# Performance work log

Hardware: AMD Instinct MI355X
Metric: run time of the kernel (lower is better)

The kernel has to match this reference:

```python
import jax, jax.numpy as jnp
import numpy as np
from jax import lax

B, S, T = 64, 64, 32
VE = VD = 32000
E = H = 256
L = 2


def _cell(x, h, c, Wih, Whh, b):
    # PyTorch LSTM gate order: i, f, g, o
    g = x @ Wih.T + h @ Whh.T + b  # [B, 4H]
    i, f, gg, o = jnp.split(g, 4, axis=-1)
    c2 = jax.nn.sigmoid(f) * c + jax.nn.sigmoid(i) * jnp.tanh(gg)
    h2 = jax.nn.sigmoid(o) * jnp.tanh(c2)
    return h2, c2


def _stack_step(x, h, c, Wih, Whh, b):
    # x: [B, E]; h, c: [L, B, H]. Stacked LSTM, dropout is identity at inference.
    hs, cs = [], []
    inp = x
    for l in range(h.shape[0]):
        h2, c2 = _cell(inp, h[l], c[l], Wih[l], Whh[l], b[l])
        hs.append(h2); cs.append(c2)
        inp = h2
    return jnp.stack(hs), jnp.stack(cs), inp


def _encode(tokens, emb, Wih, Whh, b):
    x = emb[tokens]  # [B, S, E]
    bsz = tokens.shape[0]
    h0 = jnp.zeros((L, bsz, H), x.dtype)
    c0 = jnp.zeros((L, bsz, H), x.dtype)

    def step(carry, xt):
        h, c = carry
        h, c, _ = _stack_step(xt, h, c, Wih, Whh, b)
        return (h, c), None

    (h, c), _ = lax.scan(step, (h0, c0), x.transpose(1, 0, 2))
    return h, c


def setup_inputs():
    key = jax.random.key(0)
    ks = jax.random.split(key, 12)
    sd = lambda k, shape: (jax.random.normal(k, shape, dtype=jnp.float32) * 0.05)
    return {
        "input_seq": jax.random.randint(ks[0], (B, S), 0, VE),
        "target_seq": jax.random.randint(ks[1], (B, T), 0, VD),
        "enc_emb": sd(ks[2], (VE, E)),
        "dec_emb": sd(ks[3], (VD, E)),
        "enc_Wih": sd(ks[4], (L, 4 * H, E)),
        "enc_Whh": sd(ks[5], (L, 4 * H, H)),
        "enc_b": sd(ks[6], (L, 4 * H)),
        "dec_Wih": sd(ks[7], (L, 4 * H, E)),
        "dec_Whh": sd(ks[8], (L, 4 * H, H)),
        "dec_b": sd(ks[9], (L, 4 * H)),
        "W_out": sd(ks[10], (VD, H)),
        "b_out": sd(ks[11], (VD,)),
    }


def reference(input_seq, target_seq, enc_emb, dec_emb, enc_Wih, enc_Whh, enc_b,
              dec_Wih, dec_Whh, dec_b, W_out, b_out):
    h, c = _encode(input_seq, enc_emb, enc_Wih, enc_Whh, enc_b)
    bsz, tlen = target_seq.shape
    # dec_in buffer; position 0 is BOS token target_seq[:, 0]; rest filled greedily
    buf0 = jnp.zeros((bsz, tlen), dtype=target_seq.dtype).at[:, 0].set(target_seq[:, 0])
    pos = jnp.arange(tlen)

    def outer(carry, t):
        h, c, buf = carry
        x = dec_emb[buf]  # [B, T, E] -- whole growing prefix re-fed, as in source

        def inner(carry, inp):
            hh, cc = carry
            xt, p = inp
            h2, c2, _ = _stack_step(xt, hh, cc, dec_Wih, dec_Whh, dec_b)
            m = p <= t  # only positions up to current prefix length update state
            hh = jnp.where(m, h2, hh)
            cc = jnp.where(m, c2, cc)
            return (hh, cc), None

        (h, c), _ = lax.scan(inner, (h, c), (x.transpose(1, 0, 2), pos))
        out_top = h[-1]  # LSTM output at last real position t
        pred = out_top @ W_out.T + b_out  # [B, V]
        nxt = jnp.argmax(pred, axis=-1).astype(buf.dtype)
        buf = buf.at[:, t + 1].set(nxt)
        return (h, c, buf), pred

    (_, _, _), preds = lax.scan(outer, (h, c, buf0), jnp.arange(tlen - 1))
    return preds.transpose(1, 0, 2)  # [B, T-1, V]
```

## Files before the change

kernel.cpp:

```cpp
#include <hip/hip_runtime.h>
#include <math.h>


#define B     64
#define SLEN  64
#define TLEN  32
#define HID   256
#define EMBD  256
#define G4    1024
#define VOC   32000
#define NPRED 31

typedef unsigned long long u64;

__device__ __forceinline__ float sigf(float x){ return 1.0f/(1.0f+__expf(-x)); }

__device__ __forceinline__ void gstoref(float* p, float v){
  __hip_atomic_store(p, v, __ATOMIC_RELAXED, __HIP_MEMORY_SCOPE_AGENT);
}
__device__ __forceinline__ void gstorei(int* p, int v){
  __hip_atomic_store(p, v, __ATOMIC_RELAXED, __HIP_MEMORY_SCOPE_AGENT);
}
__device__ __forceinline__ float gloadf(const float* p){
  return __hip_atomic_load(p, __ATOMIC_RELAXED, __HIP_MEMORY_SCOPE_AGENT);
}
__device__ __forceinline__ int gload32(const int* p){
  return __hip_atomic_load(p, __ATOMIC_RELAXED, __HIP_MEMORY_SCOPE_AGENT);
}

__global__ void k_init(const int* __restrict__ tgt, int* __restrict__ buf){
  int r = threadIdx.x;
  if (r < B) buf[r*TLEN] = tgt[r*TLEN];
}

__global__ void k_zero(int* __restrict__ p){
  if (threadIdx.x < 192) p[threadIdx.x] = 0;
}

__global__ __launch_bounds__(256) void k_tr(const float* __restrict__ src,
                                            float* __restrict__ dst){
  __shared__ float t[64][65];
  const int r0 = blockIdx.x*64, c0 = blockIdx.y*64;
  const int lr = threadIdx.x>>6, lc = threadIdx.x&63;
  #pragma unroll
  for (int i=0;i<16;i++){
    int r = lr + i*4;
    t[r][lc] = src[(size_t)(r0+r)*256 + c0+lc];
  }
  __syncthreads();
  #pragma unroll
  for (int i=0;i<16;i++){
    int c = lr + i*4;
    dst[(size_t)(c0+c)*1024 + r0+lc] = t[lc][c];
  }
}

__global__ __launch_bounds__(256) void k_xproj(
    const int* __restrict__ tok, int tok_stride, int pos0,
    const float* __restrict__ emb, const float* __restrict__ W,
    const float* __restrict__ b0, float* __restrict__ out)
{
  __shared__ float xT[128][64];
  const int tid  = threadIdx.x;
  const int lane = tid & 63;
  const int wv   = __builtin_amdgcn_readfirstlane(tid >> 6);
  const int pos  = pos0 + blockIdx.y;
  const int jbase= blockIdx.x*32 + wv*8;

  const int rS = tid >> 2, klane = tid & 3;
  const int tokrow = tok[rS*tok_stride + pos];
  const float* xsrc = emb + (size_t)tokrow*EMBD;

  float acc[8];
  #pragma unroll
  for (int jj=0;jj<8;jj++) acc[jj]=0.f;

  for (int c=0;c<2;c++){
    __syncthreads();
    #pragma unroll
    for (int i=0;i<32;i++){
      int k = klane + 4*i;
      xT[k][rS] = xsrc[c*128 + k];
    }
    __syncthreads();
    for (int kc=0;kc<8;kc++){
      float x[16];
      #pragma unroll
      for (int i=0;i<16;i++) x[i] = xT[kc*16+i][lane];
      #pragma unroll
      for (int jj=0;jj<8;jj++){
        const float* Wp = W + (size_t)(jbase+jj)*EMBD + c*128 + kc*16;
        float s = 0.f;
        #pragma unroll
        for (int i=0;i<16;i++) s += Wp[i]*x[i];
        acc[jj] += s;
      }
    }
  }
  #pragma unroll
  for (int jj=0;jj<8;jj++){
    int j = jbase+jj;
    out[((size_t)pos*G4 + j)*64 + lane] = acc[jj] + b0[j];
  }
}

__device__ __forceinline__ float4 dotpart(const float4* __restrict__ Wq,
                                          const float* __restrict__ hs,
                                          int kq, int jg){
  float ax=0.f, ay=0.f, az=0.f, aw=0.f;
  const float4* __restrict__ hq = (const float4*)(hs + (kq<<6));
  const float4* __restrict__ w  = Wq + (size_t)(kq<<6)*256 + jg;
  #pragma unroll 4
  for (int kk=0; kk<16; ++kk){
    float4 h4 = hq[kk];
    float4 w0 = w[0];
    float4 w1 = w[256];
    float4 w2 = w[512];
    float4 w3 = w[768];
    ax += w0.x*h4.x; ay += w0.y*h4.x; az += w0.z*h4.x; aw += w0.w*h4.x;
    ax += w1.x*h4.y; ay += w1.y*h4.y; az += w1.z*h4.y; aw += w1.w*h4.y;
    ax += w2.x*h4.z; ay += w2.y*h4.z; az += w2.z*h4.z; aw += w2.w*h4.z;
    ax += w3.x*h4.w; ay += w3.y*h4.w; az += w3.z*h4.w; aw += w3.w*h4.w;
    w += 1024;
  }
  return make_float4(ax,ay,az,aw);
}

__global__ __launch_bounds__(1024) void k_pipe(
    const float* __restrict__ xp, int nsteps,
    const float* __restrict__ WT0, const float* __restrict__ WT1i,
    const float* __restrict__ WT1h, const float* __restrict__ b1,
    float* __restrict__ h0P, float* __restrict__ h1P,
    float* __restrict__ c0P, float* __restrict__ c1P,
    float* __restrict__ h0R, float* __restrict__ p1R,
    int* __restrict__ fA, int* __restrict__ fB1, int* __restrict__ fB2,
    int fbase, int initzero)
{
  __shared__ __align__(16) float part[4][4096];
  __shared__ float xps[1024];
  __shared__ __align__(16) float hloc[256];
  __shared__ float padL[4096];
  const int tid  = threadIdx.x;
  const int kq   = tid >> 8, jg = tid & 255;
  const int role = blockIdx.x >> 6;
  const int r    = blockIdx.x & 63;
  if (nsteps < 0){ padL[tid] = xp[tid]; h0R[tid] = padL[tid ^ 1]; }

  if (role == 0){
    float c0 = 0.f;
    if (tid < HID){
      if (initzero){ c0 = 0.f; hloc[tid] = 0.f; }
      else { c0 = c0P[tid*64 + r]; hloc[tid] = h0P[tid*64 + r]; }
    }
    __syncthreads();
    const float4* W4 = (const float4*)WT0;
    for (int q = 0; q < nsteps; ++q){
      float xv = xp[((size_t)q*G4 + tid)*64 + r];
      if (tid == 0 && q >= 4){
        int tgt = fbase + q - 3, g = 0;
        while (gload32(fB1 + r) < tgt && ++g < (1<<24)) {}
      }
      xps[tid] = xv;
      float4 a = dotpart(W4, hloc, kq, jg);
      *(float4*)&part[kq][jg<<2] = a;
      __syncthreads();
      if (tid < HID){
        float g0 = part[0][tid]+part[1][tid]+part[2][tid]+part[3][tid] + xps[tid];
        float g1 = part[0][HID+tid]+part[1][HID+tid]+part[2][HID+tid]+part[3][HID+tid] + xps[HID+tid];
        float g2 = part[0][2*HID+tid]+part[1][2*HID+tid]+part[2][2*HID+tid]+part[3][2*HID+tid] + xps[2*HID+tid];
        float g3 = part[0][3*HID+tid]+part[1][3*HID+tid]+part[2][3*HID+tid]+part[3][3*HID+tid] + xps[3*HID+tid];
        c0 = sigf(g1)*c0 + sigf(g0)*tanhf(g2);
        float h = sigf(g3)*tanhf(c0);
        hloc[tid] = h;
        gstoref(h0R + (q&3)*16384 + r*256 + tid, h);
        asm volatile("s_waitcnt vmcnt(0)" ::: "memory");
      }
      __syncthreads();
      if (tid == 0) gstorei(fA + r, fbase + q + 1);
    }
    if (tid < HID){ c0P[tid*64 + r] = c0; h0P[tid*64 + r] = hloc[tid]; }
  }
  else if (role == 1){
    const float4* W4 = (const float4*)WT1i;
    for (int q = 0; q < nsteps; ++q){
      if (tid == 0){
        int tgt = fbase + q + 1, g = 0;
        while (gload32(fA + r) < tgt && ++g < (1<<24)) {}
        if (q >= 4){
          int t2 = fbase + q - 3; g = 0;
          while (gload32(fB2 + r) < t2 && ++g < (1<<24)) {}
        }
      }
      __syncthreads();
      if (tid < HID) hloc[tid] = gloadf(h0R + (q&3)*16384 + r*256 + tid);
      __syncthreads();
      float4 a = dotpart(W4, hloc, kq, jg);
      *(float4*)&part[kq][jg<<2] = a;
      __syncthreads();
      float p = part[0][tid]+part[1][tid]+part[2][tid]+part[3][tid];
      gstoref(p1R + (q&3)*65536 + r*1024 + tid, p);
      asm volatile("s_waitcnt vmcnt(0)" ::: "memory");
      __syncthreads();
      if (tid == 0) gstorei(fB1 + r, fbase + q + 1);
    }
  }
  else {
    float c1 = 0.f, bb0=0.f, bb1=0.f, bb2=0.f, bb3=0.f;
    if (tid < HID){
      bb0 = b1[tid]; bb1 = b1[HID+tid]; bb2 = b1[2*HID+tid]; bb3 = b1[3*HID+tid];
      if (initzero){ c1 = 0.f; hloc[tid] = 0.f; }
      else { c1 = c1P[tid*64 + r]; hloc[tid] = h1P[tid*64 + r]; }
    }
    __syncthreads();
    const float4* W4 = (const float4*)WT1h;
    for (int q = 0; q < nsteps; ++q){
      if (tid == 0){
        int tgt = fbase + q + 1, g = 0;
        while (gload32(fB1 + r) < tgt && ++g < (1<<24)) {}
      }
      __syncthreads();
      xps[tid] = gloadf(p1R + (q&3)*65536 + r*1024 + tid);
      asm volatile("s_waitcnt vmcnt(0)" ::: "memory");
      __syncthreads();
      if (tid == 0) gstorei(fB2 + r, fbase + q + 1);
      float4 a = dotpart(W4, hloc, kq, jg);
      *(float4*)&part[kq][jg<<2] = a;
      __syncthreads();
      if (tid < HID){
        float g0 = part[0][tid]+part[1][tid]+part[2][tid]+part[3][tid] + xps[tid] + bb0;
        float g1 = part[0][HID+tid]+part[1][HID+tid]+part[2][HID+tid]+part[3][HID+tid] + xps[HID+tid] + bb1;
        float g2 = part[0][2*HID+tid]+part[1][2*HID+tid]+part[2][2*HID+tid]+part[3][2*HID+tid] + xps[2*HID+tid] + bb2;
        float g3 = part[0][3*HID+tid]+part[1][3*HID+tid]+part[2][3*HID+tid]+part[3][3*HID+tid] + xps[3*HID+tid] + bb3;
        c1 = sigf(g1)*c1 + sigf(g0)*tanhf(g2);
        float h = sigf(g3)*tanhf(c1);
        hloc[tid] = h;
        if (q == nsteps-1) h1P[tid*64 + r] = h;
      }
      __syncthreads();
    }
    if (tid < HID) c1P[tid*64 + r] = c1;
  }
}

__global__ __launch_bounds__(256) void k_pred(
    const float* __restrict__ h1, const float* __restrict__ Wout,
    const float* __restrict__ bout, float* __restrict__ dout, int t,
    float* __restrict__ pval, int* __restrict__ pidx)
{
  __shared__ float xT[128][64];
  __shared__ float cval[4][64];
  __shared__ int   cidx[4][64];
  const int tid  = threadIdx.x;
  const int lane = tid & 63;
  const int wv   = __builtin_amdgcn_readfirstlane(tid >> 6);
  const int vbase= blockIdx.x*32 + wv*8;

  float acc[8];
  #pragma unroll
  for (int vv=0;vv<8;vv++) acc[vv]=0.f;

  for (int c=0;c<2;c++){
    __syncthreads();
    {
      const float4* s4 = (const float4*)(h1 + c*8192);
      float4* d4 = (float4*)&xT[0][0];
      #pragma unroll
      for (int i=0;i<8;i++) d4[tid + i*256] = s4[tid + i*256];
    }
    __syncthreads();
    for (int kc=0;kc<8;kc++){
      float x[16];
      #pragma unroll
      for (int i=0;i<16;i++) x[i] = xT[kc*16+i][lane];
      #pragma unroll
      for (int vv=0;vv<8;vv++){
        const float* Wp = Wout + (size_t)(vbase+vv)*HID + c*128 + kc*16;
        float s = 0.f;
        #pragma unroll
        for (int i=0;i<16;i++) s += Wp[i]*x[i];
        acc[vv] += s;
      }
    }
  }

  const int r = lane;
  float best = -INFINITY; int bi = 0;
  #pragma unroll
  for (int vv=0; vv<8; vv++){
    int v = vbase + vv;
    float val = acc[vv] + bout[v];
    dout[((size_t)r*NPRED + t)*VOC + v] = val;
    if (val > best){ best = val; bi = v; }
  }
  cval[wv][lane] = best; cidx[wv][lane] = bi;
  __syncthreads();
  if (tid < 64){
    float bb = cval[0][tid]; int bbi = cidx[0][tid];
    #pragma unroll
    for (int w=1; w<4; w++){
      float v = cval[w][tid];
      if (v > bb){ bb = v; bbi = cidx[w][tid]; }
    }
    pval[(size_t)tid*1024 + blockIdx.x] = bb;
    pidx[(size_t)tid*1024 + blockIdx.x] = bbi;
  }
}

__global__ __launch_bounds__(256) void k_amax(
    const float* __restrict__ pval, const int* __restrict__ pidx,
    int* __restrict__ buf, int t)
{
  __shared__ float sv[256]; __shared__ int si[256];
  const int r = blockIdx.x, tid = threadIdx.x;
  float best = -INFINITY; int bi = 0x7fffffff;
  for (int w = tid; w < 1000; w += 256){
    float v = pval[(size_t)r*1024 + w]; int ii = pidx[(size_t)r*1024 + w];
    if (v > best || (v == best && ii < bi)){ best = v; bi = ii; }
  }
  sv[tid] = best; si[tid] = bi;
  __syncthreads();
  for (int s2 = 128; s2 > 0; s2 >>= 1){
    if (tid < s2){
      float v = sv[tid+s2]; int ii = si[tid+s2];
      if (v > sv[tid] || (v == sv[tid] && ii < si[tid])){ sv[tid]=v; si[tid]=ii; }
    }
    __syncthreads();
  }
  if (tid == 0) buf[r*TLEN + t + 1] = si[0];
}

extern "C" void kernel_launch(void* const* d_in, const int* in_sizes, int n_in,
                              void* d_out, int out_size, void* d_ws, size_t ws_size,
                              hipStream_t stream)
{
  const int*   input_seq  = (const int*)d_in[0];
  const int*   target_seq = (const int*)d_in[1];
  const float* enc_emb = (const float*)d_in[2];
  const float* dec_emb = (const float*)d_in[3];
  const float* enc_Wih = (const float*)d_in[4];
  const float* enc_Whh = (const float*)d_in[5];
  const float* enc_b   = (const float*)d_in[6];
  const float* dec_Wih = (const float*)d_in[7];
  const float* dec_Whh = (const float*)d_in[8];
  const float* dec_b   = (const float*)d_in[9];
  const float* W_out   = (const float*)d_in[10];
  const float* b_out   = (const float*)d_in[11];
  float* out = (float*)d_out;

  float* ws   = (float*)d_ws;
  float* xp_e = ws;
  float* xp_d = xp_e + (size_t)SLEN*G4*64;
  float* h0P  = xp_d + (size_t)TLEN*G4*64;
  float* h1P  = h0P + HID*64;
  float* c0P  = h1P + HID*64;
  float* c1P  = c0P + HID*64;
  float* h0R  = c1P + HID*64;
  float* p1R  = h0R + 4*64*HID;
  float* pval = p1R + 4*64*G4;
  int*   pidx = (int*)(pval + (size_t)B*1024);
  int*   buf  = pidx + (size_t)B*1024;
  int*   fA   = buf + B*TLEN;
  int*   fB1  = fA + 64;
  int*   fB2  = fB1 + 64;
  float* WT0  = (float*)(fB2 + 64);
  float* WT1i = WT0  + HID*G4;
  float* WT1h = WT1i + HID*G4;

  k_init<<<1, 64, 0, stream>>>(target_seq, buf);
  k_zero<<<1, 256, 0, stream>>>(fA);

  dim3 trg(16, 4);
  k_tr<<<trg, 256, 0, stream>>>(enc_Whh,                   WT0);
  k_tr<<<trg, 256, 0, stream>>>(enc_Wih + (size_t)G4*EMBD, WT1i);
  k_tr<<<trg, 256, 0, stream>>>(enc_Whh + (size_t)G4*HID,  WT1h);
  k_xproj<<<dim3(32, SLEN), 256, 0, stream>>>(input_seq, SLEN, 0, enc_emb,
        enc_Wih, enc_b, xp_e);
  k_pipe<<<192, 1024, 0, stream>>>(xp_e, SLEN,
        WT0, WT1i, WT1h, enc_b + G4,
        h0P, h1P, c0P, c1P, h0R, p1R, fA, fB1, fB2, 0, 1);

  k_tr<<<trg, 256, 0, stream>>>(dec_Whh,                   WT0);
  k_tr<<<trg, 256, 0, stream>>>(dec_Wih + (size_t)G4*EMBD, WT1i);
  k_tr<<<trg, 256, 0, stream>>>(dec_Whh + (size_t)G4*HID,  WT1h);

  int fb = SLEN;
  for (int t = 0; t < NPRED; t++){
    k_xproj<<<dim3(32, 1), 256, 0, stream>>>(buf, TLEN, t, dec_emb,
        dec_Wih, dec_b, xp_d);
    k_pipe<<<192, 1024, 0, stream>>>(xp_d, t+1,
        WT0, WT1i, WT1h, dec_b + G4,
        h0P, h1P, c0P, c1P, h0R, p1R, fA, fB1, fB2, fb, 0);
    fb += t + 1;
    k_pred<<<1000, 256, 0, stream>>>(h1P, W_out, b_out, out, t, pval, pidx);
    k_amax<<<B, 256, 0, stream>>>(pval, pidx, buf, t);
  }
}
```

Baseline: 8.604 ms.

## Fuse entire greedy decode loop into one persistent multi-role kernel

Replaces the per-step host loop of xproj, pipe, pred and argmax launches with a single persistent kernel of 256 blocks split into four roles (layer-0 cell, layer-1 input projection, layer-1 cell, vocab projection with argmax and next-token embedding projection). The roles synchronise through global flag counters and ring buffers. This removes about 124 kernel launches and their serialisation, and lets the vocab projection for step t overlap with the recurrent work of step t+1. The cost is that vocab work now runs on 64 blocks instead of 1000, spin-wait synchronisation adds latency and deadlock risk, and all 256 large blocks must be co-resident.

```diff
diff --git a/kernel.cpp b/kernel.cpp
--- a/kernel.cpp
+++ b/kernel.cpp
@@ -10,6 +10,7 @@
 #define G4    1024
 #define VOC   32000
 #define NPRED 31
+#define FBASE 64
 
 typedef unsigned long long u64;
 
@@ -28,13 +29,8 @@
   return __hip_atomic_load(p, __ATOMIC_RELAXED, __HIP_MEMORY_SCOPE_AGENT);
 }
 
-__global__ void k_init(const int* __restrict__ tgt, int* __restrict__ buf){
-  int r = threadIdx.x;
-  if (r < B) buf[r*TLEN] = tgt[r*TLEN];
-}
-
 __global__ void k_zero(int* __restrict__ p){
-  if (threadIdx.x < 192) p[threadIdx.x] = 0;
+  p[threadIdx.x] = 0;
 }
 
 __global__ __launch_bounds__(256) void k_tr(const float* __restrict__ src,
@@ -242,91 +238,294 @@
   }
 }
 
-__global__ __launch_bounds__(256) void k_pred(
-    const float* __restrict__ h1, const float* __restrict__ Wout,
-    const float* __restrict__ bout, float* __restrict__ dout, int t,
-    float* __restrict__ pval, int* __restrict__ pidx)
+__global__ __launch_bounds__(1024) void k_megadec(
+    float* xp,
+    const float* __restrict__ WT0, const float* __restrict__ WT1i,
+    const float* __restrict__ WT1h, const float* __restrict__ b1,
+    const float* __restrict__ Wih0, const float* __restrict__ b0,
+    const float* __restrict__ emb,
+    const float* __restrict__ Wout, const float* __restrict__ bout,
+    float* __restrict__ dout,
+    const float* __restrict__ h0P, const float* __restrict__ h1P,
+    const float* __restrict__ c0P, const float* __restrict__ c1P,
+    float* __restrict__ h0R, float* __restrict__ p1R, float* __restrict__ h1R,
+    float* __restrict__ pPv, int* __restrict__ pPi, float* __restrict__ xeG,
+    int* __restrict__ flags)
 {
-  __shared__ float xT[128][64];
-  __shared__ float cval[4][64];
-  __shared__ int   cidx[4][64];
+  __shared__ __align__(16) float part[4][4096];
+  __shared__ float xps[1024];
+  __shared__ __align__(16) float hloc[256];
+  __shared__ int   iscr[1024];
+  __shared__ float htp[256*65];
+
+  int* fA = flags;        int* fB1 = flags + 64;  int* fB2 = flags + 128;
+  int* fH = flags + 192;  int* fP  = flags + 256; int* fX  = flags + 320;
+  int* fT = flags + 384;
+
   const int tid  = threadIdx.x;
   const int lane = tid & 63;
   const int wv   = __builtin_amdgcn_readfirstlane(tid >> 6);
-  const int vbase= blockIdx.x*32 + wv*8;
-
-  float acc[8];
-  #pragma unroll
-  for (int vv=0;vv<8;vv++) acc[vv]=0.f;
-
-  for (int c=0;c<2;c++){
+  const int kq   = tid >> 8, jg = tid & 255;
+  const int role = blockIdx.x >> 6;
+  const int r    = blockIdx.x & 63;
+
+  if (role == 0){
+    float c0 = 0.f;
+    if (tid < HID){ c0 = c0P[tid*64 + r]; hloc[tid] = h0P[tid*64 + r]; }
     __syncthreads();
-    {
-      const float4* s4 = (const float4*)(h1 + c*8192);
-      float4* d4 = (float4*)&xT[0][0];
-      #pragma unroll
-      for (int i=0;i<8;i++) d4[tid + i*256] = s4[tid + i*256];
+    const float4* W4 = (const float4*)WT0;
+    int cum = 0;
+    for (int t = 0; t < NPRED; ++t)
+    for (int p = 0; p <= t; ++p, ++cum){
+      if (wv == 0){
+        if (lane == 0 && cum >= 4){
+          int tgt = FBASE + cum - 3, g = 0;
+          while (gload32(fB1 + r) < tgt && ++g < (1<<24)) {}
+        }
+        if (p == t && t >= 1){
+          int g = 0;
+          while (!__all(gload32(fX + lane) >= t) && ++g < (1<<24)) {}
+        }
+      }
+      __syncthreads();
+      float xv = gloadf(xp + ((size_t)p*G4 + tid)*64 + r);
+      xps[tid] = xv;
+      float4 a = dotpart(W4, hloc, kq, jg);
+      *(float4*)&part[kq][jg<<2] = a;
+      __syncthreads();
+      if (tid < HID){
+        float g0 = part[0][tid]+part[1][tid]+part[2][tid]+part[3][tid] + xps[tid];
+        float g1 = part[0][HID+tid]+part[1][HID+tid]+part[2][HID+tid]+part[3][HID+tid] + xps[HID+tid];
+        float g2 = part[0][2*HID+tid]+part[1][2*HID+tid]+part[2][2*HID+tid]+part[3][2*HID+tid] + xps[2*HID+tid];
+        float g3 = part[0][3*HID+tid]+part[1][3*HID+tid]+part[2][3*HID+tid]+part[3][3*HID+tid] + xps[3*HID+tid];
+        c0 = sigf(g1)*c0 + sigf(g0)*tanhf(g2);
+        float h = sigf(g3)*tanhf(c0);
+        hloc[tid] = h;
+        gstoref(h0R + (cum&3)*16384 + r*256 + tid, h);
+        asm volatile("s_waitcnt vmcnt(0)" ::: "memory");
+      }
+      __syncthreads();
+      if (tid == 0) gstorei(fA + r, FBASE + cum + 1);
+    }
+  }
+  else if (role == 1){
+    const float4* W4 = (const float4*)WT1i;
+    int cum = 0;
+    for (int t = 0; t < NPRED; ++t)
+    for (int p = 0; p <= t; ++p, ++cum){
+      if (tid == 0){
+        int tgt = FBASE + cum + 1, g = 0;
+        while (gload32(fA + r) < tgt && ++g < (1<<24)) {}
+        if (cum >= 4){
+          int t2 = FBASE + cum - 3; g = 0;
+          while (gload32(fB2 + r) < t2 && ++g < (1<<24)) {}
+        }
+      }
+      __syncthreads();
+      if (tid < HID) hloc[tid] = gloadf(h0R + (cum&3)*16384 + r*256 + tid);
+      __syncthreads();
+      float4 a = dotpart(W4, hloc, kq, jg);
+      *(float4*)&part[kq][jg<<2] = a;
+      __syncthreads();
+      float pp = part[0][tid]+part[1][tid]+part[2][tid]+part[3][tid];
+      gstoref(p1R + (cum&3)*65536 + r*1024 + tid, pp);
+      asm volatile("s_waitcnt vmcnt(0)" ::: "memory");
+      __syncthreads();
+      if (tid == 0) gstorei(fB1 + r, FBASE + cum + 1);
+    }
+  }
+  else if (role == 2){
+    float c1 = 0.f, bb0=0.f, bb1=0.f, bb2=0.f, bb3=0.f;
+    if (tid < HID){
+      bb0 = b1[tid]; bb1 = b1[HID+tid]; bb2 = b1[2*HID+tid]; bb3 = b1[3*HID+tid];
+      c1 = c1P[tid*64 + r]; hloc[tid] = h1P[tid*64 + r];
     }
     __syncthreads();
-    for (int kc=0;kc<8;kc++){
-      float x[16];
-      #pragma unroll
-      for (int i=0;i<16;i++) x[i] = xT[kc*16+i][lane];
-      #pragma unroll
-      for (int vv=0;vv<8;vv++){
-        const float* Wp = Wout + (size_t)(vbase+vv)*HID + c*128 + kc*16;
-        float s = 0.f;
+    const float4* W4 = (const float4*)WT1h;
+    int cum = 0;
+    for (int t = 0; t < NPRED; ++t)
+    for (int p = 0; p <= t; ++p, ++cum){
+      if (tid == 0){
+        int tgt = FBASE + cum + 1, g = 0;
+        while (gload32(fB1 + r) < tgt && ++g < (1<<24)) {}
+      }
+      __syncthreads();
+      xps[tid] = gloadf(p1R + (cum&3)*65536 + r*1024 + tid);
+      asm volatile("s_waitcnt vmcnt(0)" ::: "memory");
+      __syncthreads();
+      if (tid == 0) gstorei(fB2 + r, FBASE + cum + 1);
+      float4 a = dotpart(W4, hloc, kq, jg);
+      *(float4*)&part[kq][jg<<2] = a;
+      __syncthreads();
+      if (tid < HID){
+        float g0 = part[0][tid]+part[1][tid]+part[2][tid]+part[3][tid] + xps[tid] + bb0;
+        float g1 = part[0][HID+tid]+part[1][HID+tid]+part[2][HID+tid]+part[3][HID+tid] + xps[HID+tid] + bb1;
+        float g2 = part[0][2*HID+tid]+part[1][2*HID+tid]+part[2][2*HID+tid]+part[3][2*HID+tid] + xps[2*HID+tid] + bb2;
+        float g3 = part[0][3*HID+tid]+part[1][3*HID+tid]+part[2][3*HID+tid]+part[3][3*HID+tid] + xps[3*HID+tid] + bb3;
+        c1 = sigf(g1)*c1 + sigf(g0)*tanhf(g2);
+        float h = sigf(g3)*tanhf(c1);
+        hloc[tid] = h;
+      }
+      __syncthreads();
+      if (p == t){
+        if (tid == 0 && t >= 2){
+          int g = 0;
+          while (gload32(fT) < t - 1 && ++g < (1<<24)) {}
+        }
+        __syncthreads();
+        if (tid < HID){
+          gstoref(h1R + (t&1)*16384 + r*256 + tid, hloc[tid]);
+          asm volatile("s_waitcnt vmcnt(0)" ::: "memory");
+        }
+        __syncthreads();
+        if (tid == 0) gstorei(fH + r, t + 1);
+      }
+    }
+  }
+  else {
+    const int v  = r;
+    const int v0 = v * 500;
+    const int jl = tid >> 6;
+    const float b0v = b0[v*16 + jl];
+
+    for (int t = 0; t < NPRED; ++t){
+      if (wv == 0){
+        int g = 0;
+        while (!__all(gload32(fH + lane) >= t+1) && ++g < (1<<24))
+          __builtin_amdgcn_s_sleep(4);
+      }
+      if (tid == 0 && t >= 2){
+        int g = 0;
+        while (gload32(fT) < t - 1 && ++g < (1<<24)) {}
+      }
+      __syncthreads();
+      {
+        const float* src = h1R + (size_t)(t&1)*16384;
         #pragma unroll
-        for (int i=0;i<16;i++) s += Wp[i]*x[i];
-        acc[vv] += s;
-      }
-    }
-  }
-
-  const int r = lane;
-  float best = -INFINITY; int bi = 0;
-  #pragma unroll
-  for (int vv=0; vv<8; vv++){
-    int v = vbase + vv;
-    float val = acc[vv] + bout[v];
-    dout[((size_t)r*NPRED + t)*VOC + v] = val;
-    if (val > best){ best = val; bi = v; }
-  }
-  cval[wv][lane] = best; cidx[wv][lane] = bi;
-  __syncthreads();
-  if (tid < 64){
-    float bb = cval[0][tid]; int bbi = cidx[0][tid];
-    #pragma unroll
-    for (int w=1; w<4; w++){
-      float v = cval[w][tid];
-      if (v > bb){ bb = v; bbi = cidx[w][tid]; }
-    }
-    pval[(size_t)tid*1024 + blockIdx.x] = bb;
-    pidx[(size_t)tid*1024 + blockIdx.x] = bbi;
-  }
-}
-
-__global__ __launch_bounds__(256) void k_amax(
-    const float* __restrict__ pval, const int* __restrict__ pidx,
-    int* __restrict__ buf, int t)
-{
-  __shared__ float sv[256]; __shared__ int si[256];
-  const int r = blockIdx.x, tid = threadIdx.x;
-  float best = -INFINITY; int bi = 0x7fffffff;
-  for (int w = tid; w < 1000; w += 256){
-    float v = pval[(size_t)r*1024 + w]; int ii = pidx[(size_t)r*1024 + w];
-    if (v > best || (v == best && ii < bi)){ best = v; bi = ii; }
-  }
-  sv[tid] = best; si[tid] = bi;
-  __syncthreads();
-  for (int s2 = 128; s2 > 0; s2 >>= 1){
-    if (tid < s2){
-      float v = sv[tid+s2]; int ii = si[tid+s2];
-      if (v > sv[tid] || (v == sv[tid] && ii < si[tid])){ sv[tid]=v; si[tid]=ii; }
-    }
-    __syncthreads();
-  }
-  if (tid == 0) buf[r*TLEN + t + 1] = si[0];
+        for (int i=0;i<16;i++){
+          int idx = tid + i*1024;
+          float vl = gloadf(src + idx);
+          htp[(idx & 255)*65 + (idx >> 8)] = vl;
+        }
+      }
+      __syncthreads();
+      float best = -INFINITY; int bi = 0x7fffffff;
+      for (int ib = 0; ib < 4; ++ib){
+        float acc[8];
+        #pragma unroll
+        for (int jj=0;jj<8;jj++){
+          int i = ib*8+jj;
+          acc[jj] = (wv + 16*i < 500) ? bout[v0 + wv + 16*i] : 0.f;
+        }
+        for (int kc = 0; kc < 16; ++kc){
+          float x[16];
+          #pragma unroll
+          for (int u=0;u<16;u++) x[u] = htp[(kc*16+u)*65 + lane];
+          #pragma unroll
+          for (int jj=0;jj<8;jj++){
+            int i = ib*8+jj;
+            if (wv + 16*i < 500){
+              const float* Wp = Wout + (size_t)(v0 + wv + 16*i)*HID + kc*16;
+              #pragma unroll
+              for (int u=0;u<16;u++) acc[jj] += Wp[u]*x[u];
+            }
+          }
+        }
+        #pragma unroll
+        for (int jj=0;jj<8;jj++){
+          int i = ib*8+jj;
+          if (wv + 16*i < 500){
+            int vv = v0 + wv + 16*i;
+            dout[((size_t)lane*NPRED + t)*VOC + vv] = acc[jj];
+            if (acc[jj] > best){ best = acc[jj]; bi = vv; }
+          }
+        }
+      }
+      xps[wv*64 + lane] = best; iscr[wv*64 + lane] = bi;
+      __syncthreads();
+      if (wv == 0){
+        float bb = xps[lane]; int bbi = iscr[lane];
+        #pragma unroll
+        for (int w=1; w<16; w++){
+          float vl = xps[w*64+lane]; int ii = iscr[w*64+lane];
+          if (vl > bb || (vl == bb && ii < bbi)){ bb = vl; bbi = ii; }
+        }
+        gstoref(pPv + (t&1)*4096 + v*64 + lane, bb);
+        gstorei(pPi + (t&1)*4096 + v*64 + lane, bbi);
+        asm volatile("s_waitcnt vmcnt(0)" ::: "memory");
+      }
+      __syncthreads();
+      if (tid == 0) gstorei(fP + v, t + 1);
+      if (t == NPRED-1) continue;
+
+      if (v == 0){
+        if (wv == 0){
+          int g = 0;
+          while (!__all(gload32(fP + lane) >= t+1) && ++g < (1<<24)) {}
+        }
+        __syncthreads();
+        {
+          float bb = -INFINITY; int bbi = 0x7fffffff;
+          #pragma unroll
+          for (int i=0;i<4;i++){
+            int vs = wv*4 + i;
+            float vl = gloadf(pPv + (t&1)*4096 + vs*64 + lane);
+            int  ii  = gload32(pPi + (t&1)*4096 + vs*64 + lane);
+            if (vl > bb || (vl == bb && ii < bbi)){ bb = vl; bbi = ii; }
+          }
+          xps[wv*64+lane] = bb; iscr[wv*64+lane] = bbi;
+        }
+        __syncthreads();
+        if (wv == 0){
+          float bb = xps[lane]; int bbi = iscr[lane];
+          #pragma unroll
+          for (int w=1; w<16; w++){
+            float vl = xps[w*64+lane]; int ii = iscr[w*64+lane];
+            if (vl > bb || (vl == bb && ii < bbi)){ bb = vl; bbi = ii; }
+          }
+          iscr[lane] = bbi;
+        }
+        __syncthreads();
+        {
+          int tk = iscr[tid & 63];
+          int rr = tid & 63, kb = (tid >> 6) * 16;
+          const float* er = emb + (size_t)tk*EMBD + kb;
+          #pragma unroll
+          for (int i=0;i<16;i++) gstoref(xeG + (kb+i)*64 + rr, er[i]);
+          asm volatile("s_waitcnt vmcnt(0)" ::: "memory");
+        }
+        __syncthreads();
+        if (tid == 0) gstorei(fT, t + 1);
+      }
+
+      if (tid == 0){
+        int g = 0;
+        while (gload32(fT) < t + 1 && ++g < (1<<24))
+          __builtin_amdgcn_s_sleep(2);
+      }
+      __syncthreads();
+      {
+        #pragma unroll
+        for (int i=0;i<16;i++){
+          int idx = tid + i*1024;
+          htp[(idx >> 6)*65 + (idx & 63)] = gloadf(xeG + idx);
+        }
+      }
+      __syncthreads();
+      {
+        int rr = tid & 63;
+        int j  = v*16 + jl;
+        const float* Wj = Wih0 + (size_t)j*EMBD;
+        float acc = b0v;
+        #pragma unroll 16
+        for (int k=0;k<256;k++) acc += Wj[k]*htp[k*65 + rr];
+        gstoref(xp + ((size_t)(t+1)*G4 + j)*64 + rr, acc);
+        asm volatile("s_waitcnt vmcnt(0)" ::: "memory");
+      }
+      __syncthreads();
+      if (tid == 0) gstorei(fX + v, t + 1);
+    }
+  }
 }
 
 extern "C" void kernel_launch(void* const* d_in, const int* in_sizes, int n_in,
@@ -355,19 +554,17 @@
   float* c0P  = h1P + HID*64;
   float* c1P  = c0P + HID*64;
   float* h0R  = c1P + HID*64;
-  float* p1R  = h0R + 4*64*HID;
-  float* pval = p1R + 4*64*G4;
-  int*   pidx = (int*)(pval + (size_t)B*1024);
-  int*   buf  = pidx + (size_t)B*1024;
-  int*   fA   = buf + B*TLEN;
-  int*   fB1  = fA + 64;
-  int*   fB2  = fB1 + 64;
-  float* WT0  = (float*)(fB2 + 64);
+  float* p1R  = h0R + 4*16384;
+  float* h1R  = p1R + 4*65536;
+  float* pPv  = h1R + 2*16384;
+  int*   pPi  = (int*)(pPv + 2*4096);
+  float* xeG  = (float*)(pPi + 2*4096);
+  int*   flags= (int*)(xeG + 16384);
+  float* WT0  = (float*)(flags + 512);
   float* WT1i = WT0  + HID*G4;
   float* WT1h = WT1i + HID*G4;
 
-  k_init<<<1, 64, 0, stream>>>(target_seq, buf);
-  k_zero<<<1, 256, 0, stream>>>(fA);
+  k_zero<<<1, 512, 0, stream>>>(flags);
 
   dim3 trg(16, 4);
   k_tr<<<trg, 256, 0, stream>>>(enc_Whh,                   WT0);
@@ -377,21 +574,18 @@
         enc_Wih, enc_b, xp_e);
   k_pipe<<<192, 1024, 0, stream>>>(xp_e, SLEN,
         WT0, WT1i, WT1h, enc_b + G4,
-        h0P, h1P, c0P, c1P, h0R, p1R, fA, fB1, fB2, 0, 1);
+        h0P, h1P, c0P, c1P, h0R, p1R,
+        flags, flags + 64, flags + 128, 0, 1);
 
   k_tr<<<trg, 256, 0, stream>>>(dec_Whh,                   WT0);
   k_tr<<<trg, 256, 0, stream>>>(dec_Wih + (size_t)G4*EMBD, WT1i);
   k_tr<<<trg, 256, 0, stream>>>(dec_Whh + (size_t)G4*HID,  WT1h);
-
-  int fb = SLEN;
-  for (int t = 0; t < NPRED; t++){
-    k_xproj<<<dim3(32, 1), 256, 0, stream>>>(buf, TLEN, t, dec_emb,
+  k_xproj<<<dim3(32, 1), 256, 0, stream>>>(target_seq, TLEN, 0, dec_emb,
         dec_Wih, dec_b, xp_d);
-    k_pipe<<<192, 1024, 0, stream>>>(xp_d, t+1,
+
+  k_megadec<<<256, 1024, 0, stream>>>(xp_d,
         WT0, WT1i, WT1h, dec_b + G4,
-        h0P, h1P, c0P, c1P, h0R, p1R, fA, fB1, fB2, fb, 0);
-    fb += t + 1;
-    k_pred<<<1000, 256, 0, stream>>>(h1P, W_out, b_out, out, t, pval, pidx);
-    k_amax<<<B, 256, 0, stream>>>(pval, pidx, buf, t);
-  }
-}
+        dec_Wih, dec_b, dec_emb, W_out, b_out, out,
+        h0P, h1P, c0P, c1P,
+        h0R, p1R, h1R, pPv, pPi, xeG, flags);
+}
```

After: 9.091 ms. +5.7%, slower.
